# Kernel tuning notes

Hardware: AMD Instinct MI355X
Metric: run time of the kernel (lower is better)

## Reference

```python
import jax, jax.numpy as jnp
import numpy as np

B, C, H, W = 2, 256, 48, 48
NUM_HEADS = 8
HEAD_DIM = C // NUM_HEADS
SCALE = HEAD_DIM ** (-0.5)


def setup_inputs() -> dict:
    key = jax.random.key(0)
    ks = jax.random.split(key, 5)
    s = 1.0 / np.sqrt(C)  # conv1x1 fan-in scaling
    return {
        "x": jax.random.normal(ks[0], (B, C, H, W), jnp.float32),
        "Wq": jax.random.normal(ks[1], (C, C), jnp.float32) * s,
        "bq": jnp.zeros((C,), jnp.float32),
        "Wk": jax.random.normal(ks[2], (C, C), jnp.float32) * s,
        "bk": jnp.zeros((C,), jnp.float32),
        "Wv": jax.random.normal(ks[3], (C, C), jnp.float32) * s,
        "bv": jnp.zeros((C,), jnp.float32),
        "Wo": jax.random.normal(ks[4], (C, C), jnp.float32) * s,
        "bo": jnp.zeros((C,), jnp.float32),
    }


def _proj(x, Wf, bf):
    # conv1x1: [B,C,H,W] x [Cout,Cin] -> [B,Cout,H,W]
    return jnp.einsum('bchw,oc->bohw', x, Wf) + bf[None, :, None, None]


def reference(x, Wq, bq, Wk, bk, Wv, bv, Wo, bo):
    b, c, h, w = x.shape
    n = h * w
    # projections then split heads: [B, heads, N, head_dim]
    def to_heads(t):
        return t.reshape(b, NUM_HEADS, HEAD_DIM, n).transpose(0, 1, 3, 2)
    q = to_heads(_proj(x, Wq, bq))
    k = to_heads(_proj(x, Wk, bk))
    v = to_heads(_proj(x, Wv, bv))
    attn = jnp.einsum('bhnd,bhmd->bhnm', q, k) * SCALE
    attn = jax.nn.softmax(attn, axis=-1)  # max-subtract + softmax (stable)
    out = jnp.einsum('bhnm,bhmd->bhnd', attn, v)
    out = out.transpose(0, 1, 3, 2).reshape(b, c, h, w)
    return _proj(out, Wo, bo)
```

## Files before the change

### kernel.cpp

```cpp
#include <hip/hip_runtime.h>
#include <hip/hip_bf16.h>

#define BATCH 2
#define CH 256
#define NH 8
#define HD 32
#define NPOS 2304
#define SCALE 0.17677669529663687f
#define QSCALE 0.25503482f
#define NSPLIT 3
#define KSPAN (NPOS / NSPLIT)
#define NT (KSPAN / 128)
#define QT (NPOS / 16)

typedef __attribute__((ext_vector_type(8))) short short8;
typedef __attribute__((ext_vector_type(4))) short short4e;
typedef __attribute__((ext_vector_type(4))) float f32x4;
typedef __attribute__((ext_vector_type(4))) unsigned int u32x4;

__device__ __forceinline__ unsigned short f2bf(float f) {
    unsigned int u = __builtin_bit_cast(unsigned int, f);
    u += 0x7FFFu + ((u >> 16) & 1u);
    return (unsigned short)(u >> 16);
}

__device__ __forceinline__ unsigned int cvt_pk_bf16(float a, float b) {
    unsigned int r;
    asm("v_cvt_pk_bf16_f32 %0, %1, %2" : "=v"(r) : "v"(a), "v"(b));
    return r;
}

__device__ __forceinline__ float fast_exp2(float x) {
    float r;
    asm("v_exp_f32 %0, %1" : "=v"(r) : "v"(x));
    return r;
}

#define GLOAD_LDS16(gsrc, ldst) \
    __builtin_amdgcn_global_load_lds( \
        (const __attribute__((address_space(1))) void*)(gsrc), \
        (__attribute__((address_space(3))) void*)(ldst), 16, 0, 0)

__global__ __launch_bounds__(256) void prep(
    const float* __restrict__ Wq, const float* __restrict__ Wk,
    const float* __restrict__ Wv, const float* __restrict__ Wo,
    const float* __restrict__ x,
    unsigned short* __restrict__ wbf, unsigned short* __restrict__ xT)
{
    __shared__ float Ts[32][33];
    int id = blockIdx.x;
    int t = threadIdx.x;
    if (id < 256) {
        int which = id >> 6;
        const float* src = (which == 0) ? Wq : (which == 1) ? Wk : (which == 2) ? Wv : Wo;
        unsigned short* d = wbf + (size_t)which * CH * CH;
        int i = ((id & 63) * 256 + t) * 4;
        f32x4 v = *(const f32x4*)&src[i];
        short4e o;
        #pragma unroll
        for (int j = 0; j < 4; ++j) o[j] = (short)f2bf(v[j]);
        *(short4e*)&d[i] = o;
    } else {
        int tid = id - 256;
        int b = tid / 576;
        int rem = tid % 576;
        int c0 = (rem / 72) * 32;
        int n0 = (rem % 72) * 32;
        int col = t & 31, row = t >> 5;
        #pragma unroll
        for (int i = 0; i < 4; ++i)
            Ts[row + i * 8][col] = x[((size_t)b * CH + c0 + row + i * 8) * NPOS + n0 + col];
        __syncthreads();
        #pragma unroll
        for (int i = 0; i < 4; ++i)
            xT[((size_t)b * NPOS + n0 + row + i * 8) * CH + c0 + col] = f2bf(Ts[col][row + i * 8]);
    }
}

__global__ __launch_bounds__(256) void qkv_gemm(
    const unsigned short* __restrict__ xT,
    const unsigned short* __restrict__ Wb,
    const float* __restrict__ bq, const float* __restrict__ bk,
    const float* __restrict__ bv,
    unsigned short* __restrict__ qout, unsigned short* __restrict__ kout,
    unsigned short* __restrict__ vout)
{
    int b = blockIdx.z;
    int n0 = blockIdx.x * 64;
    int o0 = blockIdx.y * 32;
    int t = threadIdx.x, w = t >> 6, lane = t & 63;
    int lo = lane & 15, hi = lane >> 4;
    int ob = o0 + (w & 1) * 16;
    int nb = n0 + (w >> 1) * 32;

    const unsigned short* Wq = Wb;
    const unsigned short* Wk = Wb + (size_t)CH * CH;
    const unsigned short* Wv = Wb + (size_t)2 * CH * CH;
    const unsigned short* xb = xT + ((size_t)b * NPOS + nb) * CH;

    f32x4 aq[2] = {}, ak[2] = {}, av[2] = {};

    for (int k0 = 0; k0 < CH; k0 += 32) {
        short8 wqf = *(const short8*)&Wq[(size_t)(ob + lo) * CH + k0 + hi * 8];
        short8 wkf = *(const short8*)&Wk[(size_t)(ob + lo) * CH + k0 + hi * 8];
        short8 wvf = *(const short8*)&Wv[(size_t)(ob + lo) * CH + k0 + hi * 8];
        #pragma unroll
        for (int g = 0; g < 2; ++g) {
            short8 xf = *(const short8*)&xb[(size_t)(g * 16 + lo) * CH + k0 + hi * 8];
            aq[g] = __builtin_amdgcn_mfma_f32_16x16x32_bf16(wqf, xf, aq[g], 0, 0, 0);
            ak[g] = __builtin_amdgcn_mfma_f32_16x16x32_bf16(wkf, xf, ak[g], 0, 0, 0);
            av[g] = __builtin_amdgcn_mfma_f32_16x16x32_bf16(wvf, xf, av[g], 0, 0, 0);
        }
    }

    int h = ob >> 5;
    int olow = (ob & 31) + hi * 4;
    #pragma unroll
    for (int g = 0; g < 2; ++g) {
        int n = nb + g * 16 + lo;
        size_t qkbase = ((size_t)(b * NH + h) * NPOS + n) * HD + olow;
        short4e pq, pk;
        #pragma unroll
        for (int r = 0; r < 4; ++r) {
            int o = ob + hi * 4 + r;
            pq[r] = (short)f2bf((aq[g][r] + bq[o]) * QSCALE);
            pk[r] = (short)f2bf(ak[g][r] + bk[o]);
        }
        *(short4e*)&qout[qkbase] = pq;
        *(short4e*)&kout[qkbase] = pk;

        int off = n & 127;
        int G = off >> 4;
        int his = lo >> 2, rr = lo & 3;
        int pi;
        if (G < 4) {
            pi = G * 32 + his * 8 + rr;
        } else {
            int gam = G & 3;
            pi = (his >= 2) ? (gam * 32 + (his - 2) * 8 + 4 + rr)
                            : ((gam ^ 1) * 32 + (his + 2) * 8 + 4 + rr);
        }
        int nperm = (n & ~127) | pi;
        size_t vbase = ((size_t)(b * NH + h) * HD + olow) * NPOS + nperm;
        #pragma unroll
        for (int r = 0; r < 4; ++r)
            vout[vbase + (size_t)r * NPOS] = f2bf(av[g][r] + bv[ob + hi * 4 + r]);
    }
}

__global__ __launch_bounds__(256) void attn_split(
    const unsigned short* __restrict__ Q,
    const unsigned short* __restrict__ K,
    const unsigned short* __restrict__ V,
    float* __restrict__ Opart,
    float* __restrict__ Lpart)
{
    const int N = NPOS;
    int xb_ = blockIdx.x;
    int bh = xb_ & 15;
    int split = xb_ >> 4;
    int w = threadIdx.x >> 6;
    int qt = blockIdx.y * 4 + w;
    int n0 = qt * 16;
    int lane = threadIdx.x & 63;
    int lo = lane & 15, hi = lane >> 4;
    bool upperhalf = lane >= 32;

    __shared__ unsigned short Ks[2][128 * HD];
    __shared__ unsigned short Vs[2][HD * 128];

    short8 qa = *(const short8*)(Q + ((size_t)bh * N + n0 + lo) * HD + hi * 8);

    const unsigned short* Kb = K + (size_t)bh * N * HD;
    const unsigned short* Vb = V + (size_t)bh * HD * N;

    short8 ones;
    #pragma unroll
    for (int j = 0; j < 8; ++j) ones[j] = (short)0x3F80;

    f32x4 oacc[2] = {{0.f,0.f,0.f,0.f},{0.f,0.f,0.f,0.f}};
    f32x4 lacc = {0.f,0.f,0.f,0.f};

    const int kbeg = split * KSPAN;

    auto stage = [&](int b, int k0) {
        #pragma unroll
        for (int j = 0; j < 2; ++j) {
            int L = w * 128 + j * 64 + lane;
            int row = L >> 2, blk = L & 3;
            const unsigned short* src = Kb + (size_t)(k0 + row) * HD + (blk ^ (row & 3)) * 8;
            GLOAD_LDS16(src, &Ks[b][(size_t)(w * 128 + j * 64) * 8]);
        }
        #pragma unroll
        for (int j = 0; j < 2; ++j) {
            int L = w * 128 + j * 64 + lane;
            int row = L >> 4, blk = L & 15;
            const unsigned short* src = Vb + (size_t)row * N + k0 + (blk ^ (row & 15)) * 8;
            GLOAD_LDS16(src, &Vs[b][(size_t)(w * 128 + j * 64) * 8]);
        }
    };

    stage(0, kbeg);
    __syncthreads();

    int buf = 0;
    #pragma unroll
    for (int kt = 0; kt < NT; ++kt) {
        int k0 = kbeg + kt * 128;
        if (kt + 1 < NT) stage(buf ^ 1, k0 + 128);

        f32x4 s[8];
        __builtin_amdgcn_s_setprio(1);
        #pragma unroll
        for (int g = 0; g < 8; ++g) {
            short8 kf = *(const short8*)&Ks[buf][(g * 16 + lo) * HD + (hi ^ (lo & 3)) * 8];
            s[g] = __builtin_amdgcn_mfma_f32_16x16x32_bf16(kf, qa, (f32x4){0.f,0.f,0.f,0.f}, 0, 0, 0);
        }
        __builtin_amdgcn_s_setprio(0);

        #pragma unroll
        for (int g = 0; g < 8; ++g)
            #pragma unroll
            for (int r = 0; r < 4; ++r)
                s[g][r] = fast_exp2(s[g][r]);

        unsigned int pk0[8], pk1[8];
        #pragma unroll
        for (int g = 0; g < 8; ++g) {
            pk0[g] = cvt_pk_bf16(s[g][0], s[g][1]);
            pk1[g] = cvt_pk_bf16(s[g][2], s[g][3]);
        }

        __builtin_amdgcn_s_setprio(1);
        #pragma unroll
        for (int c = 0; c < 4; ++c) {
            unsigned int z0 = upperhalf ? pk0[4 + c] : pk0[4 + (c ^ 1)];
            unsigned int z1 = upperhalf ? pk1[4 + c] : pk1[4 + (c ^ 1)];
            unsigned int r0 = (unsigned int)__shfl_xor((int)z0, 32);
            unsigned int r1 = (unsigned int)__shfl_xor((int)z1, 32);
            u32x4 fv = {pk0[c], pk1[c], r0, r1};
            short8 frag = __builtin_bit_cast(short8, fv);

            lacc = __builtin_amdgcn_mfma_f32_16x16x32_bf16(frag, ones, lacc, 0, 0, 0);
            #pragma unroll
            for (int df = 0; df < 2; ++df) {
                short8 vf = *(const short8*)&Vs[buf][(df * 16 + lo) * 128 + ((c * 4 + hi) ^ lo) * 8];
                oacc[df] = __builtin_amdgcn_mfma_f32_16x16x32_bf16(frag, vf, oacc[df], 0, 0, 0);
            }
        }
        __builtin_amdgcn_s_setprio(0);

        __syncthreads();
        buf ^= 1;
    }

    size_t tidx  = (((size_t)bh * QT + qt) * NSPLIT + split);
    float* ob = Opart + tidx * (HD * 16);
    #pragma unroll
    for (int df = 0; df < 2; ++df)
        *(f32x4*)&ob[(df * 16 + lo) * 16 + hi * 4] = oacc[df];
    if (lo == 0) {
        float* lb = Lpart + tidx * 16;
        #pragma unroll
        for (int r = 0; r < 4; ++r) lb[hi * 4 + r] = lacc[r];
    }
}

__global__ __launch_bounds__(256) void attn_merge(
    const float* __restrict__ Opart,
    const float* __restrict__ Lpart,
    unsigned short* __restrict__ omT)
{
    int bh = blockIdx.y, b = bh >> 3, h = bh & 7;
    int qt = blockIdx.x, n0 = qt * 16;
    int t = threadIdx.x;
    int d = t & 31;
    int r0 = t >> 5;
    size_t base = ((size_t)bh * QT + qt) * NSPLIT;
    #pragma unroll
    for (int i = 0; i < 2; ++i) {
        int row = r0 + i * 8;
        float osum = 0.f, lsum = 0.f;
        #pragma unroll
        for (int s = 0; s < NSPLIT; ++s) {
            osum += Opart[(base + s) * (HD * 16) + d * 16 + row];
            lsum += Lpart[(base + s) * 16 + row];
        }
        omT[((size_t)b * NPOS + n0 + row) * CH + h * HD + d] = f2bf(osum / lsum);
    }
}

__global__ __launch_bounds__(256) void wo_gemm(
    const unsigned short* __restrict__ omT,
    const unsigned short* __restrict__ Wo,
    const float* __restrict__ bo,
    float* __restrict__ out)
{
    int b = blockIdx.z;
    int n0 = blockIdx.x * 64;
    int o0 = blockIdx.y * 32;
    int t = threadIdx.x, w = t >> 6, lane = t & 63;
    int lo = lane & 15, hi = lane >> 4;
    int ob = o0 + (w & 1) * 16;
    int nb = n0 + (w >> 1) * 32;

    const unsigned short* xb = omT + ((size_t)b * NPOS + nb) * CH;

    f32x4 acc[2] = {};
    for (int k0 = 0; k0 < CH; k0 += 32) {
        short8 wf = *(const short8*)&Wo[(size_t)(ob + lo) * CH + k0 + hi * 8];
        #pragma unroll
        for (int g = 0; g < 2; ++g) {
            short8 xf = *(const short8*)&xb[(size_t)(g * 16 + lo) * CH + k0 + hi * 8];
            acc[g] = __builtin_amdgcn_mfma_f32_16x16x32_bf16(wf, xf, acc[g], 0, 0, 0);
        }
    }

    #pragma unroll
    for (int g = 0; g < 2; ++g) {
        int n = nb + g * 16 + lo;
        #pragma unroll
        for (int r = 0; r < 4; ++r) {
            int o = ob + hi * 4 + r;
            out[((size_t)b * CH + o) * NPOS + n] = acc[g][r] + bo[o];
        }
    }
}

extern "C" void kernel_launch(void* const* d_in, const int* in_sizes, int n_in,
                              void* d_out, int out_size, void* d_ws, size_t ws_size,
                              hipStream_t stream) {
    const float* x  = (const float*)d_in[0];
    const float* Wq = (const float*)d_in[1];
    const float* bq = (const float*)d_in[2];
    const float* Wk = (const float*)d_in[3];
    const float* bk = (const float*)d_in[4];
    const float* Wv = (const float*)d_in[5];
    const float* bv = (const float*)d_in[6];
    const float* Wo = (const float*)d_in[7];
    const float* bo = (const float*)d_in[8];
    float* out = (float*)d_out;

    const size_t E  = (size_t)BATCH * CH * NPOS;
    const size_t WS = (size_t)CH * CH;
    unsigned short* wbf = (unsigned short*)d_ws;
    unsigned short* xT  = wbf + 4 * WS;
    unsigned short* qb  = xT + E;
    unsigned short* kb  = qb + E;
    unsigned short* vT  = kb + E;
    float* Opart = (float*)(vT + E);
    float* Lpart = Opart + (size_t)16 * QT * NSPLIT * (HD * 16);
    unsigned short* om = xT;
    (void)ws_size; (void)in_sizes; (void)n_in; (void)out_size;

    hipLaunchKernelGGL(prep, dim3(256 + 1152), dim3(256), 0, stream,
                       Wq, Wk, Wv, Wo, x, wbf, xT);
    hipLaunchKernelGGL(qkv_gemm, dim3(NPOS / 64, CH / 32, BATCH), dim3(256), 0, stream,
                       xT, wbf, bq, bk, bv, qb, kb, vT);
    hipLaunchKernelGGL(attn_split, dim3(NSPLIT * 16, QT / 4), dim3(256), 0, stream,
                       qb, kb, vT, Opart, Lpart);
    hipLaunchKernelGGL(attn_merge, dim3(QT, BATCH * NH), dim3(256), 0, stream,
                       Opart, Lpart, om);
    hipLaunchKernelGGL(wo_gemm, dim3(NPOS / 64, CH / 32, BATCH), dim3(256), 0, stream,
                       om, wbf + 3 * WS, bo, out);
}
```

Baseline: 71.31 us.

## Shrink GEMM wave tiles, widen attention blocks to 512 threads, split QK phase

The QKV and output-projection GEMMs now give each wave a single 16x16 output tile instead of two, with a fully unrolled K loop, and the launch grid is doubled along the output dimension. The attention kernel now runs 8 waves per block with 512 threads and launch bounds (512,6), so each wave issues one K and one V staging load instead of two. Its score computation is split into two halves of four MFMAs, each followed immediately by exp and bf16 packing, to cut register pressure. The aim is more parallelism and occupancy, at the cost of less operand reuse in the GEMMs and more blocks to launch.

Result: slower. 75.71 us (+6.2%).

```diff
diff --git a/kernel.cpp b/kernel.cpp
--- a/kernel.cpp
+++ b/kernel.cpp
@@ -87,68 +87,62 @@
 {
     int b = blockIdx.z;
     int n0 = blockIdx.x * 64;
-    int o0 = blockIdx.y * 32;
+    int ob = blockIdx.y * 16;
     int t = threadIdx.x, w = t >> 6, lane = t & 63;
     int lo = lane & 15, hi = lane >> 4;
-    int ob = o0 + (w & 1) * 16;
-    int nb = n0 + (w >> 1) * 32;
+    int nb = n0 + w * 16;
 
     const unsigned short* Wq = Wb;
     const unsigned short* Wk = Wb + (size_t)CH * CH;
     const unsigned short* Wv = Wb + (size_t)2 * CH * CH;
     const unsigned short* xb = xT + ((size_t)b * NPOS + nb) * CH;
 
-    f32x4 aq[2] = {}, ak[2] = {}, av[2] = {};
-
+    f32x4 aq = {}, ak = {}, av = {};
+
+    #pragma unroll
     for (int k0 = 0; k0 < CH; k0 += 32) {
         short8 wqf = *(const short8*)&Wq[(size_t)(ob + lo) * CH + k0 + hi * 8];
         short8 wkf = *(const short8*)&Wk[(size_t)(ob + lo) * CH + k0 + hi * 8];
         short8 wvf = *(const short8*)&Wv[(size_t)(ob + lo) * CH + k0 + hi * 8];
-        #pragma unroll
-        for (int g = 0; g < 2; ++g) {
-            short8 xf = *(const short8*)&xb[(size_t)(g * 16 + lo) * CH + k0 + hi * 8];
-            aq[g] = __builtin_amdgcn_mfma_f32_16x16x32_bf16(wqf, xf, aq[g], 0, 0, 0);
-            ak[g] = __builtin_amdgcn_mfma_f32_16x16x32_bf16(wkf, xf, ak[g], 0, 0, 0);
-            av[g] = __builtin_amdgcn_mfma_f32_16x16x32_bf16(wvf, xf, av[g], 0, 0, 0);
-        }
+        short8 xf  = *(const short8*)&xb[(size_t)lo * CH + k0 + hi * 8];
+        aq = __builtin_amdgcn_mfma_f32_16x16x32_bf16(wqf, xf, aq, 0, 0, 0);
+        ak = __builtin_amdgcn_mfma_f32_16x16x32_bf16(wkf, xf, ak, 0, 0, 0);
+        av = __builtin_amdgcn_mfma_f32_16x16x32_bf16(wvf, xf, av, 0, 0, 0);
     }
 
     int h = ob >> 5;
     int olow = (ob & 31) + hi * 4;
-    #pragma unroll
-    for (int g = 0; g < 2; ++g) {
-        int n = nb + g * 16 + lo;
-        size_t qkbase = ((size_t)(b * NH + h) * NPOS + n) * HD + olow;
-        short4e pq, pk;
-        #pragma unroll
-        for (int r = 0; r < 4; ++r) {
-            int o = ob + hi * 4 + r;
-            pq[r] = (short)f2bf((aq[g][r] + bq[o]) * QSCALE);
-            pk[r] = (short)f2bf(ak[g][r] + bk[o]);
-        }
-        *(short4e*)&qout[qkbase] = pq;
-        *(short4e*)&kout[qkbase] = pk;
-
-        int off = n & 127;
-        int G = off >> 4;
-        int his = lo >> 2, rr = lo & 3;
-        int pi;
-        if (G < 4) {
-            pi = G * 32 + his * 8 + rr;
-        } else {
-            int gam = G & 3;
-            pi = (his >= 2) ? (gam * 32 + (his - 2) * 8 + 4 + rr)
-                            : ((gam ^ 1) * 32 + (his + 2) * 8 + 4 + rr);
-        }
-        int nperm = (n & ~127) | pi;
-        size_t vbase = ((size_t)(b * NH + h) * HD + olow) * NPOS + nperm;
-        #pragma unroll
-        for (int r = 0; r < 4; ++r)
-            vout[vbase + (size_t)r * NPOS] = f2bf(av[g][r] + bv[ob + hi * 4 + r]);
-    }
-}
-
-__global__ __launch_bounds__(256) void attn_split(
+    int n = nb + lo;
+    size_t qkbase = ((size_t)(b * NH + h) * NPOS + n) * HD + olow;
+    short4e pq, pk;
+    #pragma unroll
+    for (int r = 0; r < 4; ++r) {
+        int o = ob + hi * 4 + r;
+        pq[r] = (short)f2bf((aq[r] + bq[o]) * QSCALE);
+        pk[r] = (short)f2bf(ak[r] + bk[o]);
+    }
+    *(short4e*)&qout[qkbase] = pq;
+    *(short4e*)&kout[qkbase] = pk;
+
+    int off = n & 127;
+    int G = off >> 4;
+    int his = lo >> 2, rr = lo & 3;
+    int pi;
+    if (G < 4) {
+        pi = G * 32 + his * 8 + rr;
+    } else {
+        int gam = G & 3;
+        pi = (his >= 2) ? (gam * 32 + (his - 2) * 8 + 4 + rr)
+                        : ((gam ^ 1) * 32 + (his + 2) * 8 + 4 + rr);
+    }
+    int nperm = (n & ~127) | pi;
+    size_t vbase = ((size_t)(b * NH + h) * HD + olow) * NPOS + nperm;
+    #pragma unroll
+    for (int r = 0; r < 4; ++r)
+        vout[vbase + (size_t)r * NPOS] = f2bf(av[r] + bv[ob + hi * 4 + r]);
+}
+
+__global__ __launch_bounds__(512, 6) void attn_split(
     const unsigned short* __restrict__ Q,
     const unsigned short* __restrict__ K,
     const unsigned short* __restrict__ V,
@@ -160,7 +154,7 @@
     int bh = xb_ & 15;
     int split = xb_ >> 4;
     int w = threadIdx.x >> 6;
-    int qt = blockIdx.y * 4 + w;
+    int qt = blockIdx.y * 8 + w;
     int n0 = qt * 16;
     int lane = threadIdx.x & 63;
     int lo = lane & 15, hi = lane >> 4;
@@ -183,20 +177,17 @@
 
     const int kbeg = split * KSPAN;
 
-    auto stage = [&](int b, int k0) {
-        #pragma unroll
-        for (int j = 0; j < 2; ++j) {
-            int L = w * 128 + j * 64 + lane;
+    auto stage = [&](int bidx, int k0) {
+        int L = w * 64 + lane;
+        {
             int row = L >> 2, blk = L & 3;
             const unsigned short* src = Kb + (size_t)(k0 + row) * HD + (blk ^ (row & 3)) * 8;
-            GLOAD_LDS16(src, &Ks[b][(size_t)(w * 128 + j * 64) * 8]);
-        }
-        #pragma unroll
-        for (int j = 0; j < 2; ++j) {
-            int L = w * 128 + j * 64 + lane;
+            GLOAD_LDS16(src, &Ks[bidx][(size_t)(w * 64) * 8]);
+        }
+        {
             int row = L >> 4, blk = L & 15;
             const unsigned short* src = Vb + (size_t)row * N + k0 + (blk ^ (row & 15)) * 8;
-            GLOAD_LDS16(src, &Vs[b][(size_t)(w * 128 + j * 64) * 8]);
+            GLOAD_LDS16(src, &Vs[bidx][(size_t)(w * 64) * 8]);
         }
     };
 
@@ -209,26 +200,41 @@
         int k0 = kbeg + kt * 128;
         if (kt + 1 < NT) stage(buf ^ 1, k0 + 128);
 
-        f32x4 s[8];
-        __builtin_amdgcn_s_setprio(1);
-        #pragma unroll
-        for (int g = 0; g < 8; ++g) {
-            short8 kf = *(const short8*)&Ks[buf][(g * 16 + lo) * HD + (hi ^ (lo & 3)) * 8];
-            s[g] = __builtin_amdgcn_mfma_f32_16x16x32_bf16(kf, qa, (f32x4){0.f,0.f,0.f,0.f}, 0, 0, 0);
-        }
-        __builtin_amdgcn_s_setprio(0);
-
-        #pragma unroll
-        for (int g = 0; g < 8; ++g)
-            #pragma unroll
-            for (int r = 0; r < 4; ++r)
-                s[g][r] = fast_exp2(s[g][r]);
-
         unsigned int pk0[8], pk1[8];
-        #pragma unroll
-        for (int g = 0; g < 8; ++g) {
-            pk0[g] = cvt_pk_bf16(s[g][0], s[g][1]);
-            pk1[g] = cvt_pk_bf16(s[g][2], s[g][3]);
+
+        {
+            f32x4 s[4];
+            __builtin_amdgcn_s_setprio(1);
+            #pragma unroll
+            for (int g = 0; g < 4; ++g) {
+                short8 kf = *(const short8*)&Ks[buf][(g * 16 + lo) * HD + (hi ^ (lo & 3)) * 8];
+                s[g] = __builtin_amdgcn_mfma_f32_16x16x32_bf16(kf, qa, (f32x4){0.f,0.f,0.f,0.f}, 0, 0, 0);
+            }
+            __builtin_amdgcn_s_setprio(0);
+            #pragma unroll
+            for (int g = 0; g < 4; ++g) {
+                #pragma unroll
+                for (int r = 0; r < 4; ++r) s[g][r] = fast_exp2(s[g][r]);
+                pk0[g] = cvt_pk_bf16(s[g][0], s[g][1]);
+                pk1[g] = cvt_pk_bf16(s[g][2], s[g][3]);
+            }
+        }
+        {
+            f32x4 s[4];
+            __builtin_amdgcn_s_setprio(1);
+            #pragma unroll
+            for (int g = 0; g < 4; ++g) {
+                short8 kf = *(const short8*)&Ks[buf][((g + 4) * 16 + lo) * HD + (hi ^ (lo & 3)) * 8];
+                s[g] = __builtin_amdgcn_mfma_f32_16x16x32_bf16(kf, qa, (f32x4){0.f,0.f,0.f,0.f}, 0, 0, 0);
+            }
+            __builtin_amdgcn_s_setprio(0);
+            #pragma unroll
+            for (int g = 0; g < 4; ++g) {
+                #pragma unroll
+                for (int r = 0; r < 4; ++r) s[g][r] = fast_exp2(s[g][r]);
+                pk0[g + 4] = cvt_pk_bf16(s[g][0], s[g][1]);
+                pk1[g + 4] = cvt_pk_bf16(s[g][2], s[g][3]);
+            }
         }
 
         __builtin_amdgcn_s_setprio(1);
@@ -298,32 +304,26 @@
 {
     int b = blockIdx.z;
     int n0 = blockIdx.x * 64;
-    int o0 = blockIdx.y * 32;
+    int ob = blockIdx.y * 16;
     int t = threadIdx.x, w = t >> 6, lane = t & 63;
     int lo = lane & 15, hi = lane >> 4;
-    int ob = o0 + (w & 1) * 16;
-    int nb = n0 + (w >> 1) * 32;
+    int nb = n0 + w * 16;
 
     const unsigned short* xb = omT + ((size_t)b * NPOS + nb) * CH;
 
-    f32x4 acc[2] = {};
+    f32x4 acc = {};
+    #pragma unroll
     for (int k0 = 0; k0 < CH; k0 += 32) {
         short8 wf = *(const short8*)&Wo[(size_t)(ob + lo) * CH + k0 + hi * 8];
-        #pragma unroll
-        for (int g = 0; g < 2; ++g) {
-            short8 xf = *(const short8*)&xb[(size_t)(g * 16 + lo) * CH + k0 + hi * 8];
-            acc[g] = __builtin_amdgcn_mfma_f32_16x16x32_bf16(wf, xf, acc[g], 0, 0, 0);
-        }
-    }
-
-    #pragma unroll
-    for (int g = 0; g < 2; ++g) {
-        int n = nb + g * 16 + lo;
-        #pragma unroll
-        for (int r = 0; r < 4; ++r) {
-            int o = ob + hi * 4 + r;
-            out[((size_t)b * CH + o) * NPOS + n] = acc[g][r] + bo[o];
-        }
+        short8 xf = *(const short8*)&xb[(size_t)lo * CH + k0 + hi * 8];
+        acc = __builtin_amdgcn_mfma_f32_16x16x32_bf16(wf, xf, acc, 0, 0, 0);
+    }
+
+    int n = nb + lo;
+    #pragma unroll
+    for (int r = 0; r < 4; ++r) {
+        int o = ob + hi * 4 + r;
+        out[((size_t)b * CH + o) * NPOS + n] = acc[r] + bo[o];
     }
 }
 
@@ -355,12 +355,12 @@
 
     hipLaunchKernelGGL(prep, dim3(256 + 1152), dim3(256), 0, stream,
                        Wq, Wk, Wv, Wo, x, wbf, xT);
-    hipLaunchKernelGGL(qkv_gemm, dim3(NPOS / 64, CH / 32, BATCH), dim3(256), 0, stream,
+    hipLaunchKernelGGL(qkv_gemm, dim3(NPOS / 64, CH / 16, BATCH), dim3(256), 0, stream,
                        xT, wbf, bq, bk, bv, qb, kb, vT);
-    hipLaunchKernelGGL(attn_split, dim3(NSPLIT * 16, QT / 4), dim3(256), 0, stream,
+    hipLaunchKernelGGL(attn_split, dim3(NSPLIT * 16, QT / 8), dim3(512), 0, stream,
                        qb, kb, vT, Opart, Lpart);
     hipLaunchKernelGGL(attn_merge, dim3(QT, BATCH * NH), dim3(256), 0, stream,
                        Opart, Lpart, om);
-    hipLaunchKernelGGL(wo_gemm, dim3(NPOS / 64, CH / 32, BATCH), dim3(256), 0, stream,
+    hipLaunchKernelGGL(wo_gemm, dim3(NPOS / 64, CH / 16, BATCH), dim3(256), 0, stream,
                        om, wbf + 3 * WS, bo, out);
 }
```
